# Optimization experiments

Hardware: AMD Instinct MI355X
Metric: run time of the kernel (lower is better)

Reference implementation:

```python
import jax, jax.numpy as jnp
import numpy as np

N_NODES = 100000
N_EDGES = 3200000
IN_FEAT = 512
HID = 32
N_CLASSES = 10


def gcn_conv(x, W, b, src, dst, num_nodes):
    """PyG GCNConv: linear transform, then symmetric-normalized aggregation
    with self-loops. out_i = sum_{j->i} norm_ij * (x_j W) + d_i^{-1} * (x_i W) + b."""
    h = x @ W  # [N, out]
    ones = jnp.ones(src.shape[0], dtype=x.dtype)
    deg = jax.ops.segment_sum(ones, dst, num_segments=num_nodes) + 1.0  # +1 self-loop
    dinv = jax.lax.rsqrt(deg)
    norm = dinv[src] * dinv[dst]  # [E]
    msg = h[src] * norm[:, None]  # [E, out]
    agg = jax.ops.segment_sum(msg, dst, num_segments=num_nodes)
    agg = agg + h * (dinv * dinv)[:, None]  # self-loop term (norm = d^-1)
    return agg + b


def setup_inputs() -> dict:
    key = jax.random.key(0)
    ks = jax.random.split(key, 12)
    x0 = jax.random.normal(ks[0], (N_NODES, IN_FEAT), dtype=jnp.float32)
    edge_index = jax.random.randint(ks[1], (2, N_EDGES), 0, N_NODES, dtype=jnp.int64)
    batch = jnp.zeros((N_NODES,), dtype=jnp.int64)

    def glorot(k, shape):
        fan_in, fan_out = shape
        lim = jnp.sqrt(6.0 / (fan_in + fan_out)).astype(jnp.float32)
        return jax.random.uniform(k, shape, jnp.float32, -lim, lim)

    return {
        "x0": x0,
        "edge_index": edge_index,
        "batch": batch,
        "W1": glorot(ks[2], (IN_FEAT, HID)),
        "b1": jnp.zeros((HID,), jnp.float32),
        "W2": glorot(ks[3], (HID, HID)),
        "b2": jnp.zeros((HID,), jnp.float32),
        "W3": glorot(ks[4], (HID, HID)),
        "b3": jnp.zeros((HID,), jnp.float32),
        "lin1_W": glorot(ks[5], (HID, 16)),
        "lin1_b": jnp.zeros((16,), jnp.float32),
        "lin2_W": glorot(ks[6], (16, N_CLASSES)),
        "lin2_b": jnp.zeros((N_CLASSES,), jnp.float32),
    }


def reference(x0, edge_index, batch, W1, b1, W2, b2, W3, b3,
              lin1_W, lin1_b, lin2_W, lin2_b):
    src, dst = edge_index[0], edge_index[1]
    n = x0.shape[0]
    x1 = jax.nn.relu(gcn_conv(x0, W1, b1, src, dst, n))
    x2 = jax.nn.relu(gcn_conv(x1, W2, b2, src, dst, n))
    x3 = jax.nn.relu(gcn_conv(x2, W3, b3, src, dst, n))
    # NOTE: original code computes cat([x1,x2,x3]) but then uses only x3; we match that.
    x = jax.nn.relu(x3 @ lin1_W + lin1_b)
    # dropout p=0.5 is identity in eval mode
    x = x @ lin2_W + lin2_b
    return x
```

## Files before the change

### kernel.cpp

```cpp
#include <hip/hip_runtime.h>
#include <hip/hip_bf16.h>

typedef float f32x4 __attribute__((ext_vector_type(4)));

#define N_NODES 100000
#define NBUK 391
#define BSHIFT 8
#define HBLK 256

__global__ void k_detect(const int* __restrict__ ei, int* __restrict__ mode) {
    __shared__ int flag;
    if (threadIdx.x == 0) flag = 0;
    __syncthreads();
    int f = 0;
    for (int i = threadIdx.x; i < 4096; i += 256)
        if (ei[2 * i + 1] != 0) f = 1;
    if (f) flag = 1;
    __syncthreads();
    if (threadIdx.x == 0) *mode = flag;
}

__global__ __launch_bounds__(256) void k_hist(const int* __restrict__ ei,
                                              const int* __restrict__ mode,
                                              int* __restrict__ gh, int E, int chunk) {
    __shared__ int hist[NBUK];
    int tid = threadIdx.x, k = blockIdx.x;
    for (int b = tid; b < NBUK; b += 256) hist[b] = 0;
    __syncthreads();
    int m = *mode;
    int e0 = k * chunk, e1 = min(E, e0 + chunk);
    for (int e = e0 + tid; e < e1; e += 256) {
        int d = m ? ei[E + e] : ei[2 * (E + e)];
        if ((unsigned)d >= N_NODES) d = 0;
        atomicAdd(&hist[d >> BSHIFT], 1);
    }
    __syncthreads();
    for (int b = tid; b < NBUK; b += 256) gh[k * NBUK + b] = hist[b];
}

__global__ __launch_bounds__(256) void k_btot(const int* __restrict__ gh, int* __restrict__ btot) {
    __shared__ int s[256];
    int b = blockIdx.x, tid = threadIdx.x;
    s[tid] = gh[tid * NBUK + b];
    __syncthreads();
    for (int d = 128; d > 0; d >>= 1) {
        if (tid < d) s[tid] += s[tid + d];
        __syncthreads();
    }
    if (tid == 0) btot[b] = s[0];
}

__global__ void k_scan_btot(const int* __restrict__ btot, int* __restrict__ bbase,
                            int* __restrict__ rowptr, int E) {
    __shared__ int s[512];
    int tid = threadIdx.x;
    int v = (tid < NBUK) ? btot[tid] : 0;
    s[tid] = v;
    __syncthreads();
    for (int d = 1; d < 512; d <<= 1) {
        int t = (tid >= d) ? s[tid - d] : 0;
        __syncthreads();
        s[tid] += t;
        __syncthreads();
    }
    if (tid < NBUK) bbase[tid] = s[tid] - v;
    if (tid == 0) { bbase[NBUK] = E; rowptr[N_NODES] = E; }
}

__global__ __launch_bounds__(256) void k_scan_cols(int* __restrict__ gh, const int* __restrict__ bbase) {
    __shared__ int s[256];
    int b = blockIdx.x, tid = threadIdx.x;
    int v = gh[tid * NBUK + b];
    s[tid] = v;
    __syncthreads();
    for (int d = 1; d < 256; d <<= 1) {
        int t = (tid >= d) ? s[tid - d] : 0;
        __syncthreads();
        s[tid] += t;
        __syncthreads();
    }
    gh[tid * NBUK + b] = bbase[b] + s[tid] - v;
}

__global__ __launch_bounds__(256) void k_bucketize(const int* __restrict__ ei,
                                                   const int* __restrict__ mode,
                                                   const int* __restrict__ offs,
                                                   int2* __restrict__ bp, int E, int chunk) {
    __shared__ int cur[NBUK];
    int tid = threadIdx.x, k = blockIdx.x;
    for (int b = tid; b < NBUK; b += 256) cur[b] = offs[k * NBUK + b];
    __syncthreads();
    int m = *mode;
    int e0 = k * chunk, e1 = min(E, e0 + chunk);
    for (int e = e0 + tid; e < e1; e += 256) {
        int s, d;
        if (m) { s = ei[e]; d = ei[E + e]; }
        else   { s = ei[2 * e]; d = ei[2 * (E + e)]; }
        if ((unsigned)s >= N_NODES) s = 0;
        if ((unsigned)d >= N_NODES) d = 0;
        int pos = atomicAdd(&cur[d >> BSHIFT], 1);
        int2 p; p.x = s; p.y = d;
        bp[pos] = p;
    }
}

__global__ __launch_bounds__(256) void k_build_csr(const int2* __restrict__ bp,
                                                   const int* __restrict__ bbase,
                                                   int* __restrict__ rowptr,
                                                   float* __restrict__ dinv,
                                                   int* __restrict__ csr) {
    __shared__ int cnt[256];
    __shared__ int s[256];
    __shared__ int cur[256];
    int b = blockIdx.x, tid = threadIdx.x;
    int nb = b << BSHIFT;
    int estart = bbase[b], eend = bbase[b + 1];
    cnt[tid] = 0;
    __syncthreads();
    for (int e = estart + tid; e < eend; e += 256) {
        int2 p = bp[e];
        atomicAdd(&cnt[p.y - nb], 1);
    }
    __syncthreads();
    int v = cnt[tid];
    s[tid] = v;
    __syncthreads();
    for (int d = 1; d < 256; d <<= 1) {
        int t = (tid >= d) ? s[tid - d] : 0;
        __syncthreads();
        s[tid] += t;
        __syncthreads();
    }
    int excl = s[tid] - v;
    int node = nb + tid;
    if (node < N_NODES) {
        rowptr[node] = estart + excl;
        dinv[node] = rsqrtf((float)v + 1.0f);
    }
    cur[tid] = estart + excl;
    __syncthreads();
    for (int e = estart + tid; e < eend; e += 256) {
        int2 p = bp[e];
        int pos = atomicAdd(&cur[p.y - nb], 1);
        csr[pos] = p.x;
    }
}

__global__ __launch_bounds__(256) void k_gemm1(const float* __restrict__ X,
                                               const float* __restrict__ W,
                                               const float* __restrict__ dinv,
                                               float* __restrict__ H) {
    __shared__ float lds[8448];
    float* xs  = lds;
    float* wsw = lds + 4160;
    int tid = threadIdx.x;
    int row = tid & 63;
    int kc  = tid >> 6;
    long row0 = (long)blockIdx.x * 64;

    float acc[32];
#pragma unroll
    for (int c = 0; c < 32; c++) acc[c] = 0.f;

    for (int k0 = 0; k0 < 512; k0 += 64) {
        __syncthreads();
#pragma unroll
        for (int u = 0; u < 8; u++) {
            int idx = u * 256 + tid;
            wsw[idx] = W[k0 * 32 + idx];
        }
#pragma unroll
        for (int u = 0; u < 4; u++) {
            int idx = u * 256 + tid;
            int rr = idx >> 4, j = idx & 15;
            long grow = row0 + rr;
            f32x4 v = {0.f, 0.f, 0.f, 0.f};
            if (grow < N_NODES) v = *(const f32x4*)&X[grow * 512 + k0 + 4 * j];
            float* dp = &xs[rr * 65 + 4 * j];
            dp[0] = v.x; dp[1] = v.y; dp[2] = v.z; dp[3] = v.w;
        }
        __syncthreads();
        int kbase = kc * 16;
#pragma unroll
        for (int kk = 0; kk < 16; kk++) {
            float xk = xs[row * 65 + kbase + kk];
            const float* wrow = &wsw[(kbase + kk) * 32];
#pragma unroll
            for (int c = 0; c < 32; c += 4) {
                f32x4 wv = *(const f32x4*)&wrow[c];
                acc[c]     += xk * wv.x;
                acc[c + 1] += xk * wv.y;
                acc[c + 2] += xk * wv.z;
                acc[c + 3] += xk * wv.w;
            }
        }
    }
    __syncthreads();
#pragma unroll
    for (int c = 0; c < 32; c++) lds[(kc * 64 + row) * 33 + c] = acc[c];
    __syncthreads();
#pragma unroll
    for (int i = 0; i < 8; i++) {
        int o = i * 256 + tid;
        int r = o >> 5, c = o & 31;
        float sv = lds[r * 33 + c] + lds[(64 + r) * 33 + c]
                 + lds[(128 + r) * 33 + c] + lds[(192 + r) * 33 + c];
        long grow = row0 + r;
        if (grow < N_NODES) H[grow * 32 + c] = sv * dinv[grow];
    }
}

__device__ __forceinline__ float gather_sum(const float* __restrict__ Hf,
                                            const int* __restrict__ csr,
                                            int e0, int e1, int f) {
    float a0 = 0.f, a1 = 0.f, a2 = 0.f, a3 = 0.f;
    for (int base = e0; base < e1; base += 32) {
        int idx = base + f;
        int sl = (idx < e1) ? csr[idx] : 0;
        int mm = e1 - base;
        if (mm >= 32) {
#pragma unroll
            for (int j = 0; j < 32; j += 4) {
                int s0 = __shfl(sl, j, 32);
                int s1 = __shfl(sl, j + 1, 32);
                int s2 = __shfl(sl, j + 2, 32);
                int s3 = __shfl(sl, j + 3, 32);
                a0 += Hf[(long)s0 * 32];
                a1 += Hf[(long)s1 * 32];
                a2 += Hf[(long)s2 * 32];
                a3 += Hf[(long)s3 * 32];
            }
        } else {
            for (int j = 0; j < mm; j++) {
                int s0 = __shfl(sl, j, 32);
                a0 += Hf[(long)s0 * 32];
            }
        }
    }
    return (a0 + a1) + (a2 + a3);
}

__global__ __launch_bounds__(256) void k_agg_mm(const float* __restrict__ H,
                                                const int* __restrict__ rowptr,
                                                const int* __restrict__ csr,
                                                const float* __restrict__ dinv,
                                                const float* __restrict__ bias,
                                                const float* __restrict__ W,
                                                float* __restrict__ Hout, int n) {
    __shared__ float ws[1024];
    int tid = threadIdx.x;
    for (int t = tid; t < 1024; t += 256) ws[t] = W[t];
    __syncthreads();
    int node = blockIdx.x * 8 + (tid >> 5);
    int f = tid & 31;
    if (node >= n) return;
    int e0 = rowptr[node], e1 = rowptr[node + 1];
    const float* Hf = H + f;
    float asum = gather_sum(Hf, csr, e0, e1, f);
    float dv = dinv[node];
    float v = dv * (asum + Hf[(long)node * 32]) + bias[f];
    v = fmaxf(v, 0.f);
    float o = 0.f;
#pragma unroll
    for (int k = 0; k < 32; k++) {
        float vk = __shfl(v, k, 32);
        o += vk * ws[k * 32 + f];
    }
    Hout[(long)node * 32 + f] = o * dv;
}

__global__ __launch_bounds__(256) void k_agg_head(const float* __restrict__ H,
                                                  const int* __restrict__ rowptr,
                                                  const int* __restrict__ csr,
                                                  const float* __restrict__ dinv,
                                                  const float* __restrict__ bias,
                                                  const float* __restrict__ L1W,
                                                  const float* __restrict__ L1B,
                                                  const float* __restrict__ L2W,
                                                  const float* __restrict__ L2B,
                                                  float* __restrict__ out, int n) {
    __shared__ float w1[512];
    __shared__ float w2[160];
    __shared__ float bb1[16];
    __shared__ float bb2[10];
    int tid = threadIdx.x;
    for (int t = tid; t < 512; t += 256) w1[t] = L1W[t];
    if (tid < 160) w2[tid] = L2W[tid];
    if (tid < 16) bb1[tid] = L1B[tid];
    if (tid < 10) bb2[tid] = L2B[tid];
    __syncthreads();
    int node = blockIdx.x * 8 + (tid >> 5);
    int f = tid & 31;
    if (node >= n) return;
    int e0 = rowptr[node], e1 = rowptr[node + 1];
    const float* Hf = H + f;
    float asum = gather_sum(Hf, csr, e0, e1, f);
    float dv = dinv[node];
    float v = dv * (asum + Hf[(long)node * 32]) + bias[f];
    v = fmaxf(v, 0.f);
    int c1 = f & 15;
    float t1 = 0.f;
#pragma unroll
    for (int k = 0; k < 32; k++) {
        float vk = __shfl(v, k, 32);
        t1 += vk * w1[k * 16 + c1];
    }
    t1 = fmaxf(t1 + bb1[c1], 0.f);
    int c2 = (f < 10) ? f : 0;
    float o = 0.f;
#pragma unroll
    for (int k = 0; k < 16; k++) {
        float tk = __shfl(t1, k, 32);
        o += tk * w2[k * 10 + c2];
    }
    o += bb2[c2];
    if (f < 10) out[(long)node * 10 + f] = o;
}

extern "C" void kernel_launch(void* const* d_in, const int* in_sizes, int n_in,
                              void* d_out, int out_size, void* d_ws, size_t ws_size,
                              hipStream_t stream) {
    const float* x0 = (const float*)d_in[0];
    const int* ei = (const int*)d_in[1];
    const float* W1 = (const float*)d_in[3];
    const float* b1 = (const float*)d_in[4];
    const float* W2 = (const float*)d_in[5];
    const float* b2 = (const float*)d_in[6];
    const float* W3 = (const float*)d_in[7];
    const float* b3 = (const float*)d_in[8];
    const float* l1W = (const float*)d_in[9];
    const float* l1b = (const float*)d_in[10];
    const float* l2W = (const float*)d_in[11];
    const float* l2b = (const float*)d_in[12];

    const int E = in_sizes[1] / 2;
    const int N = N_NODES;

    char* w = (char*)d_ws;
    float* h      = (float*)(w);
    float* xb     = (float*)(w + 12800000);
    int2*  bp     = (int2*) (w);
    int*   gh     = (int*)  (w + 25600000);
    int*   btot   = (int*)  (w + 26000384);
    int*   bbase  = (int*)  (w + 26001948);
    int*   rowptr = (int*)  (w + 26003516);
    float* dinv   = (float*)(w + 26403532);
    int*   csr    = (int*)  (w + 26803532);
    int*   mode   = (int*)  (w + 39603532);

    const int chunk = (E + HBLK - 1) / HBLK;
    const int AGB = (N + 7) / 8;
    const int G1B = (N + 63) / 64;

    k_detect<<<1, 256, 0, stream>>>(ei, mode);
    k_hist<<<HBLK, 256, 0, stream>>>(ei, mode, gh, E, chunk);
    k_btot<<<NBUK, 256, 0, stream>>>(gh, btot);
    k_scan_btot<<<1, 512, 0, stream>>>(btot, bbase, rowptr, E);
    k_scan_cols<<<NBUK, 256, 0, stream>>>(gh, bbase);
    k_bucketize<<<HBLK, 256, 0, stream>>>(ei, mode, gh, bp, E, chunk);
    k_build_csr<<<NBUK, 256, 0, stream>>>(bp, bbase, rowptr, dinv, csr);

    k_gemm1<<<G1B, 256, 0, stream>>>(x0, W1, dinv, h);
    k_agg_mm<<<AGB, 256, 0, stream>>>(h, rowptr, csr, dinv, b1, W2, xb, N);
    k_agg_mm<<<AGB, 256, 0, stream>>>(xb, rowptr, csr, dinv, b2, W3, h, N);
    k_agg_head<<<AGB, 256, 0, stream>>>(h, rowptr, csr, dinv, b3,
                                        l1W, l1b, l2W, l2b, (float*)d_out, N);
}
```

Before: 792.2 us.

## Restructure first-layer GEMM to one row per thread with scalar W reads

The first-layer GEMM now gives each thread a whole output row across 256 rows per block, walking K in chunks of 16 staged in LDS. W is no longer staged in LDS. Its values are read straight from global memory with wave-uniform addresses, which the compiler can turn into scalar loads. This drops the cross-thread K-split reduction through LDS and the W staging, and writes output as vector stores. In exchange there are far fewer blocks (about 391), more barriers per block, and X is loaded in narrow 64-byte row segments, so memory coalescing may suffer.

Result: slower. 869.7 us (+9.8%).

```diff
diff --git a/kernel.cpp b/kernel.cpp
--- a/kernel.cpp
+++ b/kernel.cpp
@@ -146,67 +146,56 @@
     }
 }
 
+#define G1_KC 16
+#define G1_ROWS 256
 __global__ __launch_bounds__(256) void k_gemm1(const float* __restrict__ X,
                                                const float* __restrict__ W,
                                                const float* __restrict__ dinv,
                                                float* __restrict__ H) {
-    __shared__ float lds[8448];
-    float* xs  = lds;
-    float* wsw = lds + 4160;
+    __shared__ float xs[G1_ROWS * 20];
     int tid = threadIdx.x;
-    int row = tid & 63;
-    int kc  = tid >> 6;
-    long row0 = (long)blockIdx.x * 64;
+    long row0 = (long)blockIdx.x * G1_ROWS;
+    long myrow = row0 + tid;
 
     float acc[32];
 #pragma unroll
     for (int c = 0; c < 32; c++) acc[c] = 0.f;
 
-    for (int k0 = 0; k0 < 512; k0 += 64) {
-        __syncthreads();
-#pragma unroll
-        for (int u = 0; u < 8; u++) {
-            int idx = u * 256 + tid;
-            wsw[idx] = W[k0 * 32 + idx];
-        }
+    for (int k0 = 0; k0 < 512; k0 += G1_KC) {
+        __syncthreads();
 #pragma unroll
         for (int u = 0; u < 4; u++) {
             int idx = u * 256 + tid;
-            int rr = idx >> 4, j = idx & 15;
+            int rr = idx >> 2, j = idx & 3;
             long grow = row0 + rr;
             f32x4 v = {0.f, 0.f, 0.f, 0.f};
             if (grow < N_NODES) v = *(const f32x4*)&X[grow * 512 + k0 + 4 * j];
-            float* dp = &xs[rr * 65 + 4 * j];
-            dp[0] = v.x; dp[1] = v.y; dp[2] = v.z; dp[3] = v.w;
+            *(f32x4*)&xs[rr * 20 + 4 * j] = v;
         }
         __syncthreads();
-        int kbase = kc * 16;
-#pragma unroll
-        for (int kk = 0; kk < 16; kk++) {
-            float xk = xs[row * 65 + kbase + kk];
-            const float* wrow = &wsw[(kbase + kk) * 32];
-#pragma unroll
-            for (int c = 0; c < 32; c += 4) {
-                f32x4 wv = *(const f32x4*)&wrow[c];
-                acc[c]     += xk * wv.x;
-                acc[c + 1] += xk * wv.y;
-                acc[c + 2] += xk * wv.z;
-                acc[c + 3] += xk * wv.w;
+#pragma unroll
+        for (int kk = 0; kk < G1_KC; kk += 4) {
+            f32x4 xq = *(const f32x4*)&xs[tid * 20 + kk];
+            const float* wbase = &W[(long)(k0 + kk) * 32];
+#pragma unroll
+            for (int q = 0; q < 4; q++) {
+                float xk = xq[q];
+#pragma unroll
+                for (int c = 0; c < 32; c++)
+                    acc[c] = fmaf(xk, wbase[q * 32 + c], acc[c]);
             }
         }
     }
-    __syncthreads();
-#pragma unroll
-    for (int c = 0; c < 32; c++) lds[(kc * 64 + row) * 33 + c] = acc[c];
-    __syncthreads();
-#pragma unroll
-    for (int i = 0; i < 8; i++) {
-        int o = i * 256 + tid;
-        int r = o >> 5, c = o & 31;
-        float sv = lds[r * 33 + c] + lds[(64 + r) * 33 + c]
-                 + lds[(128 + r) * 33 + c] + lds[(192 + r) * 33 + c];
-        long grow = row0 + r;
-        if (grow < N_NODES) H[grow * 32 + c] = sv * dinv[grow];
+    if (myrow < N_NODES) {
+        float dv = dinv[myrow];
+        float* out = &H[myrow * 32];
+#pragma unroll
+        for (int c = 0; c < 32; c += 4) {
+            f32x4 v;
+            v.x = acc[c] * dv; v.y = acc[c + 1] * dv;
+            v.z = acc[c + 2] * dv; v.w = acc[c + 3] * dv;
+            *(f32x4*)&out[c] = v;
+        }
     }
 }
 
@@ -350,7 +339,7 @@
 
     const int chunk = (E + HBLK - 1) / HBLK;
     const int AGB = (N + 7) / 8;
-    const int G1B = (N + 63) / 64;
+    const int G1B = (N + G1_ROWS - 1) / G1_ROWS;
 
     k_detect<<<1, 256, 0, stream>>>(ei, mode);
     k_hist<<<HBLK, 256, 0, stream>>>(ei, mode, gh, E, chunk);
```
